# Optimization experiments

Hardware: AMD Instinct MI355X
Metric: run time of the kernel (lower is better)

## Reference

```python
import jax, jax.numpy as jnp
import numpy as np

GROUPS = 8
EPS = 1e-5


def setup_inputs() -> dict:
    key = jax.random.key(0)
    k1, k2, k3 = jax.random.split(key, 3)
    B, C, H, W = 4, 256, 64, 64
    x = jax.random.normal(k1, (B, C, H, W), dtype=jnp.float32)
    gamma = jnp.ones((C,), dtype=jnp.float32)
    beta = jnp.zeros((C,), dtype=jnp.float32)
    # conv1x1 weights flattened to [out, in]
    w_qkv = jax.random.normal(k2, (3 * C, C), dtype=jnp.float32) * (C ** -0.5)
    w_proj = jax.random.normal(k3, (C, C), dtype=jnp.float32) * (C ** -0.5)
    b_proj = jnp.zeros((C,), dtype=jnp.float32)
    return {"x": x, "gamma": gamma, "beta": beta, "w_qkv": w_qkv,
            "w_proj": w_proj, "b_proj": b_proj}


def group_norm(x, gamma, beta):
    B, C, H, W = x.shape
    xr = x.reshape(B, GROUPS, C // GROUPS, H * W)
    mu = xr.mean(axis=(2, 3), keepdims=True)
    var = xr.var(axis=(2, 3), keepdims=True)
    xn = (xr - mu) * jax.lax.rsqrt(var + EPS)
    xn = xn.reshape(B, C, H * W)
    return xn * gamma[None, :, None] + beta[None, :, None]


def reference(x, gamma, beta, w_qkv, w_proj, b_proj):
    B, C, H, W = x.shape
    N = H * W
    xn = group_norm(x, gamma, beta)               # [B, C, N]
    qkv = jnp.einsum('oc,bcn->bon', w_qkv, xn)    # [B, 3C, N]
    q, k, v = jnp.split(qkv, 3, axis=1)           # each [B, C, N]
    # attn[b, n, m] = sum_c q[b,c,n] * k[b,c,m] * C^-0.5
    scores = jnp.einsum('bcn,bcm->bnm', q, k) * (C ** -0.5)  # [B, N, N]
    attn = jax.nn.softmax(scores, axis=-1)
    # out = v @ attn^T  -> out[b,c,n] = sum_m v[b,c,m] * attn[b,n,m]
    out = jnp.einsum('bcm,bnm->bcn', v, attn)     # [B, C, N]
    y = jnp.einsum('oc,bcn->bon', w_proj, out) + b_proj[None, :, None]
    return x + y.reshape(B, C, H, W)
```

## Files before the change

kernel.cpp:

```cpp
#include <hip/hip_runtime.h>
#include <hip/hip_bf16.h>

#define BB 4
#define CC 256
#define NN 4096
#define GG 8
#define SPLITS 4
#define TKV 32
#define ITERS (NN / SPLITS / TKV)

typedef unsigned char u8;
typedef unsigned short u16;
typedef unsigned int u32;
typedef __bf16 b16x8 __attribute__((ext_vector_type(8)));
typedef float f32x4 __attribute__((ext_vector_type(4)));
typedef u32 u32x4 __attribute__((ext_vector_type(4)));
typedef u32 u32x2 __attribute__((ext_vector_type(2)));
typedef u16 u16x4 __attribute__((ext_vector_type(4)));
typedef int i32x8 __attribute__((ext_vector_type(8)));

#define QS 0.09016844005556021f
#define FMAX 8.0f


__device__ __forceinline__ u16 f2bf(float f) {
    u32 u = __builtin_bit_cast(u32, f);
    u = (u + 0x7FFFu + ((u >> 16) & 1u)) >> 16;
    return (u16)u;
}

__device__ __forceinline__ float bf2f(u16 h) {
    return __builtin_bit_cast(float, (u32)h << 16);
}

__device__ __forceinline__ u32 pack_bf2(float a, float b) {
    float2 f; f.x = a; f.y = b;
    __hip_bfloat162 h = __float22bfloat162_rn(f);
    u32 r;
    __builtin_memcpy(&r, &h, 4);
    return r;
}

__device__ __forceinline__ float exp2_raw(float x) {
#if __has_builtin(__builtin_amdgcn_exp2f)
    return __builtin_amdgcn_exp2f(x);
#else
    float r;
    asm("v_exp_f32 %0, %1" : "=v"(r) : "v"(x));
    return r;
#endif
}

__device__ __forceinline__ b16x8 ldfrag(const u16* p) {
    u32x4 v = *reinterpret_cast<const u32x4*>(p);
    return __builtin_bit_cast(b16x8, v);
}

__device__ __forceinline__ int pk_fp8x4(float a, float b, float c, float d) {
    int r = __builtin_amdgcn_cvt_pk_fp8_f32(a, b, 0, false);
    r = __builtin_amdgcn_cvt_pk_fp8_f32(c, d, r, true);
    return r;
}

__device__ __forceinline__ long as_long(u32x2 v) { return __builtin_bit_cast(long, v); }

__device__ __forceinline__ i32x8 cat8(u32x4 a, u32x4 b) {
    i32x8 r;
    r[0] = (int)a.x; r[1] = (int)a.y; r[2] = (int)a.z; r[3] = (int)a.w;
    r[4] = (int)b.x; r[5] = (int)b.y; r[6] = (int)b.z; r[7] = (int)b.w;
    return r;
}

__device__ __forceinline__ f32x4 mfma_qk128(i32x8 a, i32x8 b, f32x4 c) {
    return __builtin_amdgcn_mfma_scale_f32_16x16x128_f8f6f4(a, b, c, 0, 0, 0, 127, 0, 127);
}

__device__ __forceinline__ u32 swz16(u32 v) {
    return (u32)__builtin_amdgcn_ds_swizzle((int)v, 0x401F);
}

__device__ __forceinline__ void pls32(u32& a, u32& b) {
    asm("v_permlane32_swap_b32 %0, %1" : "+v"(a), "+v"(b));
}

typedef __attribute__((address_space(1))) const unsigned int* gas_p;
typedef __attribute__((address_space(3))) unsigned int* las_p;

__device__ __forceinline__ void g2l(const u8* g, u8* l) {
    __builtin_amdgcn_global_load_lds((gas_p)g, (las_p)l, 16, 0, 0);
}

__device__ __forceinline__ void g2l16(const u16* g, u16* l) {
    __builtin_amdgcn_global_load_lds((gas_p)g, (las_p)l, 16, 0, 0);
}

__global__ void fold_w(const float* __restrict__ w_qkv, const float* __restrict__ w_proj,
                       const float* __restrict__ gamma, const float* __restrict__ beta,
                       const float* __restrict__ gsum,
                       u16* __restrict__ wqf, float* __restrict__ biasq,
                       u16* __restrict__ wpf) {
    int o = blockIdx.x;
    int b = blockIdx.y;
    int c = threadIdx.x;
    int g = c >> 5;
    const float inv = 1.f / ((CC / GG) * NN);
    float s  = gsum[(b * GG + g) * 2];
    float ss = gsum[(b * GG + g) * 2 + 1];
    float mu = s * inv;
    float rstd = rsqrtf(ss * inv - mu * mu + 1e-5f);
    float a  = gamma[c] * rstd;
    float bb = beta[c] - mu * a;
    float w = w_qkv[o * CC + c];
    size_t fe = ((size_t)((o >> 4) * 8 + (c >> 5)) * 64 + ((c & 31) >> 3) * 16 + (o & 15)) * 8 + (c & 7);
    wqf[(size_t)b * 768 * CC + fe] = f2bf(w * a);
    float part = w * bb;
    #pragma unroll
    for (int off = 32; off; off >>= 1) part += __shfl_down(part, off, 64);
    __shared__ float red[4];
    if ((threadIdx.x & 63) == 0) red[threadIdx.x >> 6] = part;
    __syncthreads();
    if (threadIdx.x == 0) biasq[b * 768 + o] = red[0] + red[1] + red[2] + red[3];
    if (b == 0 && o < CC) {
        float wp = w_proj[o * CC + c];
        wpf[fe] = f2bf(wp);
    }
}

__global__ void transpose_x(const float* __restrict__ x, u16* __restrict__ xtf,
                            float* __restrict__ gsum) {
    __shared__ float tile[64][65];
    __shared__ float red[4][4];
    int n0 = blockIdx.x * 64, c0 = blockIdx.y * 64, b = blockIdx.z;
    int t = threadIdx.x;
    int c4 = (t & 15) * 4;
    int r0 = t >> 4;
    const float* xp = x + (size_t)b * CC * NN;
    float s0 = 0.f, ss0 = 0.f, s1 = 0.f, ss1 = 0.f;
    #pragma unroll
    for (int i = 0; i < 4; ++i) {
        int row = i * 16 + r0;
        float4 v = *reinterpret_cast<const float4*>(&xp[(size_t)(c0 + row) * NN + n0 + c4]);
        tile[row][c4 + 0] = v.x; tile[row][c4 + 1] = v.y;
        tile[row][c4 + 2] = v.z; tile[row][c4 + 3] = v.w;
        float s = v.x + v.y + v.z + v.w;
        float q = v.x * v.x + v.y * v.y + v.z * v.z + v.w * v.w;
        if (i < 2) { s0 += s; ss0 += q; } else { s1 += s; ss1 += q; }
    }
    #pragma unroll
    for (int off = 32; off; off >>= 1) {
        s0 += __shfl_down(s0, off, 64); ss0 += __shfl_down(ss0, off, 64);
        s1 += __shfl_down(s1, off, 64); ss1 += __shfl_down(ss1, off, 64);
    }
    int wid = t >> 6;
    if ((t & 63) == 0) { red[wid][0] = s0; red[wid][1] = ss0; red[wid][2] = s1; red[wid][3] = ss1; }
    __syncthreads();
    if (t < 2) {
        float s  = red[0][t * 2] + red[1][t * 2] + red[2][t * 2] + red[3][t * 2];
        float ss = red[0][t * 2 + 1] + red[1][t * 2 + 1] + red[2][t * 2 + 1] + red[3][t * 2 + 1];
        int g = (c0 >> 5) + t;
        atomicAdd(&gsum[(b * GG + g) * 2], s);
        atomicAdd(&gsum[(b * GG + g) * 2 + 1], ss);
    }
    int nl = t >> 2;
    int cbq = t & 3;
    int l15 = nl & 15;
    int ntile = (n0 >> 4) + (nl >> 4);
    int kk = (c0 >> 5) + (cbq >> 1);
    u16* ob = xtf + (size_t)b * NN * CC;
    #pragma unroll
    for (int g = 0; g < 4; ++g) {
        int quad = (cbq & 1) * 2 + (g >> 1);
        int j0 = (g & 1) * 4;
        u16x4 v;
        v.x = f2bf(tile[cbq * 16 + g * 4 + 0][nl]);
        v.y = f2bf(tile[cbq * 16 + g * 4 + 1][nl]);
        v.z = f2bf(tile[cbq * 16 + g * 4 + 2][nl]);
        v.w = f2bf(tile[cbq * 16 + g * 4 + 3][nl]);
        *reinterpret_cast<u16x4*>(ob + ((size_t)(ntile * 8 + kk) * 64 + quad * 16 + l15) * 8 + j0) = v;
    }
}

__global__ void __launch_bounds__(256) qkv_gemm(const u16* __restrict__ wqf,
                                                const float* __restrict__ biasq,
                                                const u16* __restrict__ xtf,
                                                u8* __restrict__ qtf, u8* __restrict__ ktf,
                                                u8* __restrict__ vvf) {
    __shared__ u16 bx[16384];
    int b = blockIdx.z;
    int o0 = blockIdx.y * 128;
    int n0 = blockIdx.x * 64;
    int lane = threadIdx.x & 63, w = threadIdx.x >> 6;
    int l15 = lane & 15, quad = lane >> 4;
    const bool isv = (o0 >= 512);
    const u16* Bg = xtf + (size_t)b * NN * CC + (size_t)n0 * 256;
    #pragma unroll
    for (int j = 0; j < 8; ++j) {
        int c = w * 8 + j;
        g2l16(Bg + (size_t)c * 512 + lane * 8, bx + (size_t)c * 512 + lane * 8);
    }
    __syncthreads();

    const u16* A = wqf + (size_t)b * 768 * CC;
    f32x4 acc[2][4] = {};
    #pragma unroll
    for (int kk = 0; kk < 8; ++kk) {
        b16x8 af[2];
        #pragma unroll
        for (int t = 0; t < 2; ++t) {
            int otile = (o0 >> 4) + w * 2 + t;
            af[t] = ldfrag(A + (size_t)(otile * 8 + kk) * 512 + lane * 8);
        }
        #pragma unroll
        for (int nt = 0; nt < 4; ++nt) {
            b16x8 bf = ldfrag(bx + (size_t)(nt * 8 + kk) * 512 + lane * 8);
            if (!isv) {
                acc[0][nt] = __builtin_amdgcn_mfma_f32_16x16x32_bf16(af[0], bf, acc[0][nt], 0, 0, 0);
                acc[1][nt] = __builtin_amdgcn_mfma_f32_16x16x32_bf16(af[1], bf, acc[1][nt], 0, 0, 0);
            } else {
                acc[0][nt] = __builtin_amdgcn_mfma_f32_16x16x32_bf16(bf, af[0], acc[0][nt], 0, 0, 0);
                acc[1][nt] = __builtin_amdgcn_mfma_f32_16x16x32_bf16(bf, af[1], acc[1][nt], 0, 0, 0);
            }
        }
    }
    if (!isv) {
        #pragma unroll
        for (int t = 0; t < 2; ++t) {
            int o_base = o0 + (w * 2 + t) * 16 + quad * 4;
            float bias[4];
            #pragma unroll
            for (int r = 0; r < 4; ++r) bias[r] = biasq[b * 768 + o_base + r];
            int oloc = (o0 < 256) ? o_base : (o_base - 256);
            u8* dst = ((o0 < 256) ? qtf : ktf) + (size_t)b * NN * CC;
            #pragma unroll
            for (int nt = 0; nt < 4; ++nt) {
                int n = n0 + nt * 16 + l15;
                int pk = pk_fp8x4(acc[t][nt][0] + bias[0], acc[t][nt][1] + bias[1],
                                  acc[t][nt][2] + bias[2], acc[t][nt][3] + bias[3]);
                size_t addr = (size_t)(n >> 4) * 4096 + (size_t)(oloc >> 7) * 2048
                            + (size_t)((oloc >> 4) & 1) * 1024
                            + (size_t)(((oloc & 127) >> 5) * 16 + (n & 15)) * 16
                            + (oloc & 15);
                *reinterpret_cast<u32*>(dst + addr) = (u32)pk;
            }
        }
    } else {
        u8* dst = vvf + (size_t)b * NN * CC;
        #pragma unroll
        for (int t = 0; t < 2; ++t) {
            int o = o0 + (w * 2 + t) * 16 + l15;
            int cb = o - 512;
            float bias_v = biasq[b * 768 + o];
            #pragma unroll
            for (int nt = 0; nt < 4; ++nt) {
                int kv0 = n0 + nt * 16 + quad * 4;
                int pk = pk_fp8x4(acc[t][nt][0] + bias_v, acc[t][nt][1] + bias_v,
                                  acc[t][nt][2] + bias_v, acc[t][nt][3] + bias_v);
                size_t addr = (size_t)((kv0 >> 5) * 8 + (cb >> 5)) * 1024
                            + ((kv0 & 31) >> 3) * 256 + (cb & 15) * 16
                            + ((cb >> 4) & 1) * 8 + (kv0 & 7);
                *reinterpret_cast<u32*>(dst + addr) = (u32)pk;
            }
        }
    }
}

__global__ void __launch_bounds__(256, 4) flash(const u8* __restrict__ qtf,
                                                const u8* __restrict__ ktf,
                                                const u8* __restrict__ vvf,
                                                u16* __restrict__ po,
                                                float* __restrict__ lp) {
    __shared__ u8 kbuf[2][8192];
    __shared__ u8 vbuf[2][8192];
    int lin = blockIdx.x;
    int chunk = lin & 15;
    int nblk = lin >> 4;
    int b = chunk >> 2, sp = chunk & 3;
    int lane = threadIdx.x & 63, w = threadIdx.x >> 6;
    int l15 = lane & 15, quad = lane >> 4;
    int ntile = nblk * 4 + w;
    const u8* kb8 = ktf + (size_t)b * NN * CC;
    const u8* vb8 = vvf + (size_t)b * NN * CC;
    const bool qodd = (quad & 1) != 0;

    i32x8 qop[2];
    {
        const u8* qp = qtf + (size_t)b * NN * CC + (size_t)ntile * 4096
                     + (size_t)lane * 16;
        u32x4 q0 = *reinterpret_cast<const u32x4*>(qp);
        u32x4 q1 = *reinterpret_cast<const u32x4*>(qp + 1024);
        u32x4 q2 = *reinterpret_cast<const u32x4*>(qp + 2048);
        u32x4 q3 = *reinterpret_cast<const u32x4*>(qp + 2048 + 1024);
        qop[0] = cat8(q0, q1);
        qop[1] = cat8(q2, q3);
    }

    f32x4 acco[16] = {};
    f32x4 accs[2];
    const f32x4 zz = {0.f, 0.f, 0.f, 0.f};
    float lsum = 0.f;

    const int m_beg = sp * (NN / SPLITS);

    auto stage_k = [&](int buf, int m0) {
        const u8* ks = kb8 + ((size_t)m0 << 8);
        #pragma unroll
        for (int j = 0; j < 2; ++j) {
            int idx = w * 2 + j;
            g2l(ks + idx * 1024 + lane * 16, &kbuf[buf][idx * 1024]);
        }
    };
    auto stage_v = [&](int buf, int m0) {
        const u8* vs = vb8 + ((size_t)m0 << 8);
        #pragma unroll
        for (int j = 0; j < 2; ++j) {
            int idx = w * 2 + j;
            g2l(vs + idx * 1024 + lane * 16, &vbuf[buf][idx * 1024]);
        }
    };
    auto qk_tile = [&](const u8* kc) {
        __builtin_amdgcn_s_setprio(1);
        const u8* kp = kc + (size_t)lane * 16;
        #pragma unroll
        for (int mm = 0; mm < 2; ++mm) {
            f32x4 acc = zz;
            #pragma unroll
            for (int cc = 0; cc < 2; ++cc) {
                const u8* p = kp + mm * 4096 + cc * 2048;
                u32x4 k0 = *reinterpret_cast<const u32x4*>(p);
                u32x4 k1 = *reinterpret_cast<const u32x4*>(p + 1024);
                acc = mfma_qk128(cat8(k0, k1), qop[cc], acc);
            }
            accs[mm] = acc;
        }
        __builtin_amdgcn_s_setprio(0);
    };
    auto exch = [&](int pa, int pb) -> long {
        u32 a = (u32)pa, bm = (u32)pb;
        u32 ax = swz16(a), bx = swz16(bm);
        pls32(a, bm);
        pls32(ax, bx);
        u32 blo = qodd ? bx : a;
        u32 bhi = qodd ? bm : ax;
        return as_long(u32x2{blo, bhi});
    };

    stage_k(0, m_beg);
    stage_v(0, m_beg);
    stage_k(1, m_beg + TKV);
    __syncthreads();
    qk_tile(&kbuf[0][0]);
    __syncthreads();

    for (int it = 0; it < ITERS; ++it) {
        int cur = it & 1;
        int pk[2];
        #pragma unroll
        for (int mm = 0; mm < 2; ++mm) {
            float e0 = exp2_raw(fmaf(accs[mm][0], QS, -FMAX));
            float e1 = exp2_raw(fmaf(accs[mm][1], QS, -FMAX));
            float e2 = exp2_raw(fmaf(accs[mm][2], QS, -FMAX));
            float e3 = exp2_raw(fmaf(accs[mm][3], QS, -FMAX));
            lsum += (e0 + e1) + (e2 + e3);
            pk[mm] = pk_fp8x4(e0, e1, e2, e3);
        }
        long bop = exch(pk[0], pk[1]);
        if (it + 1 < ITERS) qk_tile(&kbuf[cur ^ 1][0]);
        if (it + 2 < ITERS) stage_k(cur, m_beg + (it + 2) * TKV);
        if (it + 1 < ITERS) stage_v(cur ^ 1, m_beg + (it + 1) * TKV);
        const u8* vc = &vbuf[cur][0];
        __builtin_amdgcn_s_setprio(1);
        #pragma unroll
        for (int c2 = 0; c2 < 8; ++c2) {
            u32x4 vf = *reinterpret_cast<const u32x4*>(vc + (size_t)c2 * 1024 + lane * 16);
            acco[c2 * 2]     = __builtin_amdgcn_mfma_f32_16x16x32_fp8_fp8(
                as_long(u32x2{vf.x, vf.y}), bop, acco[c2 * 2], 0, 0, 0);
            acco[c2 * 2 + 1] = __builtin_amdgcn_mfma_f32_16x16x32_fp8_fp8(
                as_long(u32x2{vf.z, vf.w}), bop, acco[c2 * 2 + 1], 0, 0, 0);
        }
        __builtin_amdgcn_s_setprio(0);
        __syncthreads();
    }
    u16* pochunk = po + ((size_t)(sp * BB + b) * 256 + ntile) * 4096;
    #pragma unroll
    for (int ct = 0; ct < 16; ++ct) {
        u32x2 st;
        st.x = pack_bf2(acco[ct][0], acco[ct][1]);
        st.y = pack_bf2(acco[ct][2], acco[ct][3]);
        *reinterpret_cast<u32x2*>(pochunk + (size_t)(ct * 64 + quad * 16 + l15) * 4) = st;
    }
    lsum += __shfl_xor(lsum, 16, 64);
    lsum += __shfl_xor(lsum, 32, 64);
    if (lane < 16)
        lp[(size_t)(sp * BB + b) * NN + ntile * 16 + l15] = lsum;
}

__global__ void __launch_bounds__(512) proj(const u16* __restrict__ wpf,
                                            const float* __restrict__ b_proj,
                                            const u16* __restrict__ po,
                                            const float* __restrict__ lp,
                                            const float* __restrict__ x,
                                            float* __restrict__ out) {
    __shared__ u16 bO[16384];
    int b = blockIdx.y, n0 = blockIdx.x * 64;
    int t = threadIdx.x;
    {
        int u = t & 127, ntl = t >> 7;
        int nb = (n0 >> 4) + ntl;
        int a = u & 7;
        int cblk = u >> 3;
        float accn[2][16] = {};
        float lsum2[2] = {};
        #pragma unroll
        for (int s = 0; s < SPLITS; ++s) {
            const u16* src = po + (((size_t)(s * BB + b) * 256 + nb) * 4096)
                           + cblk * 256 + a * 8;
            #pragma unroll
            for (int q4 = 0; q4 < 4; ++q4) {
                u16 s16[8];
                *reinterpret_cast<u32x4*>(s16) = *reinterpret_cast<const u32x4*>(src + q4 * 64);
                #pragma unroll
                for (int k = 0; k < 8; ++k)
                    accn[k >> 2][q4 * 4 + (k & 3)] += bf2f(s16[k]);
            }
            lsum2[0] += lp[(size_t)(s * BB + b) * NN + nb * 16 + a * 2];
            lsum2[1] += lp[(size_t)(s * BB + b) * NN + nb * 16 + a * 2 + 1];
        }
        #pragma unroll
        for (int nsel = 0; nsel < 2; ++nsel) {
            float inv = 1.f / lsum2[nsel];
            int row = a * 2 + nsel;
            #pragma unroll
            for (int h = 0; h < 2; ++h) {
                u16 outv[8];
                #pragma unroll
                for (int j = 0; j < 8; ++j) outv[j] = f2bf(accn[nsel][h * 8 + j] * inv);
                int kk = cblk >> 1, quad_f = (cblk & 1) * 2 + h;
                size_t off = ((size_t)(ntl * 8 + kk) * 64 + quad_f * 16 + row) * 8;
                *reinterpret_cast<u32x4*>(bO + off) = *reinterpret_cast<const u32x4*>(outv);
            }
        }
    }
    __syncthreads();
    int lane = t & 63, w = t >> 6;
    int l15 = lane & 15, quad = lane >> 4;
    f32x4 acc2[2][4] = {};
    #pragma unroll
    for (int kk = 0; kk < 8; ++kk) {
        b16x8 af[2];
        #pragma unroll
        for (int tt = 0; tt < 2; ++tt) {
            int otile = w * 2 + tt;
            af[tt] = ldfrag(wpf + (size_t)(otile * 8 + kk) * 512 + lane * 8);
        }
        #pragma unroll
        for (int nt = 0; nt < 4; ++nt) {
            b16x8 bf = ldfrag(bO + (size_t)(nt * 8 + kk) * 512 + lane * 8);
            acc2[0][nt] = __builtin_amdgcn_mfma_f32_16x16x32_bf16(af[0], bf, acc2[0][nt], 0, 0, 0);
            acc2[1][nt] = __builtin_amdgcn_mfma_f32_16x16x32_bf16(af[1], bf, acc2[1][nt], 0, 0, 0);
        }
    }
    #pragma unroll
    for (int tt = 0; tt < 2; ++tt) {
        int o_base = (w * 2 + tt) * 16 + quad * 4;
        #pragma unroll
        for (int nt = 0; nt < 4; ++nt) {
            int n = n0 + nt * 16 + l15;
            #pragma unroll
            for (int r = 0; r < 4; ++r) {
                int o = o_base + r;
                size_t idx = ((size_t)(b * CC + o)) * NN + n;
                out[idx] = acc2[tt][nt][r] + b_proj[o] + x[idx];
            }
        }
    }
}

extern "C" void kernel_launch(void* const* d_in, const int* in_sizes, int n_in,
                              void* d_out, int out_size, void* d_ws, size_t ws_size,
                              hipStream_t stream) {
    const float* x      = (const float*)d_in[0];
    const float* gamma  = (const float*)d_in[1];
    const float* beta   = (const float*)d_in[2];
    const float* w_qkv  = (const float*)d_in[3];
    const float* w_proj = (const float*)d_in[4];
    const float* b_proj = (const float*)d_in[5];
    float* out = (float*)d_out;

    char* p = (char*)d_ws;
    float* gsum  = (float*)p; p += 256;
    float* biasq = (float*)p; p += (size_t)BB * 768 * sizeof(float);
    u16* wqf = (u16*)p; p += (size_t)BB * 768 * CC * 2;
    u16* wpf = (u16*)p; p += (size_t)CC * CC * 2;
    u16* xtf = (u16*)p; p += (size_t)BB * NN * CC * 2;
    u8* qtf8 = (u8*)p; p += (size_t)BB * NN * CC;
    u8* ktf8 = (u8*)p; p += (size_t)BB * NN * CC;
    u8* vvf8 = (u8*)p; p += (size_t)BB * NN * CC;
    u16* po = (u16*)p; p += (size_t)SPLITS * BB * NN * CC * 2;
    float* lp = (float*)p; p += (size_t)SPLITS * BB * NN * sizeof(float);
    (void)ws_size; (void)in_sizes; (void)n_in; (void)out_size;

    (void)hipMemsetAsync(gsum, 0, BB * GG * 2 * sizeof(float), stream);
    transpose_x<<<dim3(NN / 64, CC / 64, BB), 256, 0, stream>>>(x, xtf, gsum);
    fold_w<<<dim3(768, BB), 256, 0, stream>>>(w_qkv, w_proj, gamma, beta, gsum, wqf, biasq, wpf);
    qkv_gemm<<<dim3(NN / 64, 6, BB), 256, 0, stream>>>(wqf, biasq, xtf, qtf8, ktf8, vvf8);
    flash<<<(NN / 64) * SPLITS * BB, 256, 0, stream>>>(qtf8, ktf8, vvf8, po, lp);
    proj<<<dim3(NN / 64, BB), 512, 0, stream>>>(wpf, b_proj, po, lp, x, out);
}
```

Before: 170.1 us.

## Loop all six output chunks per QKV GEMM block to reuse staged x tile

```diff
diff --git a/kernel.cpp b/kernel.cpp
--- a/kernel.cpp
+++ b/kernel.cpp
@@ -186,12 +186,10 @@
                                                 u8* __restrict__ qtf, u8* __restrict__ ktf,
                                                 u8* __restrict__ vvf) {
     __shared__ u16 bx[16384];
-    int b = blockIdx.z;
-    int o0 = blockIdx.y * 128;
+    int b = blockIdx.y;
     int n0 = blockIdx.x * 64;
     int lane = threadIdx.x & 63, w = threadIdx.x >> 6;
     int l15 = lane & 15, quad = lane >> 4;
-    const bool isv = (o0 >= 512);
     const u16* Bg = xtf + (size_t)b * NN * CC + (size_t)n0 * 256;
     #pragma unroll
     for (int j = 0; j < 8; ++j) {
@@ -201,28 +199,26 @@
     __syncthreads();
 
     const u16* A = wqf + (size_t)b * 768 * CC;
-    f32x4 acc[2][4] = {};
-    #pragma unroll
-    for (int kk = 0; kk < 8; ++kk) {
-        b16x8 af[2];
-        #pragma unroll
-        for (int t = 0; t < 2; ++t) {
-            int otile = (o0 >> 4) + w * 2 + t;
-            af[t] = ldfrag(A + (size_t)(otile * 8 + kk) * 512 + lane * 8);
-        }
-        #pragma unroll
-        for (int nt = 0; nt < 4; ++nt) {
-            b16x8 bf = ldfrag(bx + (size_t)(nt * 8 + kk) * 512 + lane * 8);
-            if (!isv) {
+
+    #pragma unroll 1
+    for (int oc = 0; oc < 4; ++oc) {
+        int o0 = oc * 128;
+        f32x4 acc[2][4] = {};
+        #pragma unroll
+        for (int kk = 0; kk < 8; ++kk) {
+            b16x8 af[2];
+            #pragma unroll
+            for (int t = 0; t < 2; ++t) {
+                int otile = (o0 >> 4) + w * 2 + t;
+                af[t] = ldfrag(A + (size_t)(otile * 8 + kk) * 512 + lane * 8);
+            }
+            #pragma unroll
+            for (int nt = 0; nt < 4; ++nt) {
+                b16x8 bf = ldfrag(bx + (size_t)(nt * 8 + kk) * 512 + lane * 8);
                 acc[0][nt] = __builtin_amdgcn_mfma_f32_16x16x32_bf16(af[0], bf, acc[0][nt], 0, 0, 0);
                 acc[1][nt] = __builtin_amdgcn_mfma_f32_16x16x32_bf16(af[1], bf, acc[1][nt], 0, 0, 0);
-            } else {
-                acc[0][nt] = __builtin_amdgcn_mfma_f32_16x16x32_bf16(bf, af[0], acc[0][nt], 0, 0, 0);
-                acc[1][nt] = __builtin_amdgcn_mfma_f32_16x16x32_bf16(bf, af[1], acc[1][nt], 0, 0, 0);
-            }
-        }
-    }
-    if (!isv) {
+            }
+        }
         #pragma unroll
         for (int t = 0; t < 2; ++t) {
             int o_base = o0 + (w * 2 + t) * 16 + quad * 4;
@@ -243,8 +239,28 @@
                 *reinterpret_cast<u32*>(dst + addr) = (u32)pk;
             }
         }
-    } else {
-        u8* dst = vvf + (size_t)b * NN * CC;
+    }
+
+    u8* dstv = vvf + (size_t)b * NN * CC;
+    #pragma unroll 1
+    for (int oc = 4; oc < 6; ++oc) {
+        int o0 = oc * 128;
+        f32x4 acc[2][4] = {};
+        #pragma unroll
+        for (int kk = 0; kk < 8; ++kk) {
+            b16x8 af[2];
+            #pragma unroll
+            for (int t = 0; t < 2; ++t) {
+                int otile = (o0 >> 4) + w * 2 + t;
+                af[t] = ldfrag(A + (size_t)(otile * 8 + kk) * 512 + lane * 8);
+            }
+            #pragma unroll
+            for (int nt = 0; nt < 4; ++nt) {
+                b16x8 bf = ldfrag(bx + (size_t)(nt * 8 + kk) * 512 + lane * 8);
+                acc[0][nt] = __builtin_amdgcn_mfma_f32_16x16x32_bf16(bf, af[0], acc[0][nt], 0, 0, 0);
+                acc[1][nt] = __builtin_amdgcn_mfma_f32_16x16x32_bf16(bf, af[1], acc[1][nt], 0, 0, 0);
+            }
+        }
         #pragma unroll
         for (int t = 0; t < 2; ++t) {
             int o = o0 + (w * 2 + t) * 16 + l15;
@@ -258,7 +274,7 @@
                 size_t addr = (size_t)((kv0 >> 5) * 8 + (cb >> 5)) * 1024
                             + ((kv0 & 31) >> 3) * 256 + (cb & 15) * 16
                             + ((cb >> 4) & 1) * 8 + (kv0 & 7);
-                *reinterpret_cast<u32*>(dst + addr) = (u32)pk;
+                *reinterpret_cast<u32*>(dstv + addr) = (u32)pk;
             }
         }
     }
@@ -363,11 +379,11 @@
             lsum += (e0 + e1) + (e2 + e3);
             pk[mm] = pk_fp8x4(e0, e1, e2, e3);
         }
-        long bop = exch(pk[0], pk[1]);
         if (it + 1 < ITERS) qk_tile(&kbuf[cur ^ 1][0]);
         if (it + 2 < ITERS) stage_k(cur, m_beg + (it + 2) * TKV);
         if (it + 1 < ITERS) stage_v(cur ^ 1, m_beg + (it + 1) * TKV);
         const u8* vc = &vbuf[cur][0];
+        long bop = exch(pk[0], pk[1]);
         __builtin_amdgcn_s_setprio(1);
         #pragma unroll
         for (int c2 = 0; c2 < 8; ++c2) {
@@ -502,7 +518,7 @@
     (void)hipMemsetAsync(gsum, 0, BB * GG * 2 * sizeof(float), stream);
     transpose_x<<<dim3(NN / 64, CC / 64, BB), 256, 0, stream>>>(x, xtf, gsum);
     fold_w<<<dim3(768, BB), 256, 0, stream>>>(w_qkv, w_proj, gamma, beta, gsum, wqf, biasq, wpf);
-    qkv_gemm<<<dim3(NN / 64, 6, BB), 256, 0, stream>>>(wqf, biasq, xtf, qtf8, ktf8, vvf8);
+    qkv_gemm<<<dim3(NN / 64, BB), 256, 0, stream>>>(wqf, biasq, xtf, qtf8, ktf8, vvf8);
     flash<<<(NN / 64) * SPLITS * BB, 256, 0, stream>>>(qtf8, ktf8, vvf8, po, lp);
     proj<<<dim3(NN / 64, BB), 512, 0, stream>>>(wpf, b_proj, po, lp, x, out);
 }
```

Result: slower. 173.9 us (+2.2%).
